# Optimization experiments

Hardware: AMD Instinct MI355X
Metric: run time of the kernel (lower is better)

## Reference

```python
import jax, jax.numpy as jnp
import numpy as np

N_HEAD = 12

def setup_inputs() -> dict:
    key = jax.random.key(0)
    ks = jax.random.split(key, 5)
    B, T, C = 2, 2048, 768
    s = 0.02
    return {
        "x": jax.random.normal(ks[0], (B, T, C), jnp.float32),
        "c_attn_w": jax.random.normal(ks[1], (C, 3 * C), jnp.float32) * s,
        "c_attn_b": jax.random.normal(ks[2], (3 * C,), jnp.float32) * s,
        "c_proj_w": jax.random.normal(ks[3], (C, C), jnp.float32) * s,
        "c_proj_b": jax.random.normal(ks[4], (C,), jnp.float32) * s,
    }

def reference(x, c_attn_w, c_attn_b, c_proj_w, c_proj_b):
    B, T, C = x.shape
    H = N_HEAD
    D = C // H
    qkv = x @ c_attn_w + c_attn_b              # [B,T,3C]
    q, k, v = jnp.split(qkv, 3, axis=-1)
    # [B,T,C] -> [B,H,T,D]
    q = q.reshape(B, T, H, D).transpose(0, 2, 1, 3)
    k = k.reshape(B, T, H, D).transpose(0, 2, 1, 3)
    v = v.reshape(B, T, H, D).transpose(0, 2, 1, 3)
    att = jnp.einsum('bhqd,bhkd->bhqk', q, k) * (1.0 / np.sqrt(D))
    causal = jnp.tril(jnp.ones((T, T), bool))  # [T,T]
    att = jnp.where(causal[None, None], att, jnp.float32(-jnp.inf))
    att = jax.nn.softmax(att, axis=-1)
    y = jnp.einsum('bhqk,bhkd->bhqd', att, v)  # [B,H,T,D]
    y = y.transpose(0, 2, 1, 3).reshape(B, T, C)
    return y @ c_proj_w + c_proj_b
```

## Files before the change

kernel.cpp:

```cpp
#include <hip/hip_runtime.h>
#include <hip/hip_bf16.h>


using half4   = __attribute__((ext_vector_type(4))) _Float16;
using half8   = __attribute__((ext_vector_type(8))) _Float16;
using floatx4 = __attribute__((ext_vector_type(4))) float;

#define T_SEQ 2048
#define NHEAD 12
#define HDIM 64
#define C3 2304
#define CDIM 768
#define BT 4096
#define BH 24

static __device__ inline _Float16 f2h(float f) { return (_Float16)f; }

static __device__ inline void bar_lgkm() {
    __builtin_amdgcn_s_waitcnt(0xc07f);
    __builtin_amdgcn_s_barrier();
}

__global__ __launch_bounds__(256)
void prologue(const float* __restrict__ wa, const float* __restrict__ wp,
              _Float16* __restrict__ wTa, _Float16* __restrict__ wTp) {
    __shared__ float tile[32][33];
    int blk = blockIdx.x, tid = threadIdx.x;
    const float* w; _Float16* wT; int K, N, bx, by;
    if (blk < 1728) { w = wa; wT = wTa; K = CDIM; N = C3; bx = blk % 72; by = blk / 72; }
    else { int b2 = blk - 1728; w = wp; wT = wTp; K = CDIM; N = CDIM; bx = b2 % 24; by = b2 / 24; }
    int tx = tid & 31, ty = tid >> 5;
    #pragma unroll
    for (int j = 0; j < 32; j += 8) {
        int k = by * 32 + ty + j, n = bx * 32 + tx;
        tile[ty + j][tx] = w[(long)k * N + n];
    }
    __syncthreads();
    #pragma unroll
    for (int j = 0; j < 32; j += 8) {
        int nO = bx * 32 + ty + j, kO = by * 32 + tx;
        wT[(long)nO * K + kO] = f2h(tile[tx][ty + j]);
    }
}

__global__ __launch_bounds__(256)
void gemm_qkv(const float* __restrict__ X, const _Float16* __restrict__ Bt,
              const float* __restrict__ bias,
              _Float16* __restrict__ Qb, _Float16* __restrict__ Kb,
              _Float16* __restrict__ Vt) {
    __shared__ __align__(16) _Float16 As[128 * 72];
    __shared__ __align__(16) _Float16 Bs[96 * 72];
    const int K = CDIM;
    int tid = threadIdx.x;
    int m0 = blockIdx.x * 128, n0 = blockIdx.y * 96;
    int w = tid >> 6, l = tid & 63;
    int wm = (w >> 1) * 64, wn = (w & 1) * 48;
    int lr = l & 15, lq = l >> 4;

    int rs = tid >> 3, cs = (tid & 7) * 8;

    floatx4 acc[4][3] = {};

    floatx4 Arf[4][2]; half8 Br[3];
    #pragma unroll
    for (int j = 0; j < 4; ++j) {
        Arf[j][0] = *(const floatx4*)&X[(long)(m0 + j * 32 + rs) * K + cs];
        Arf[j][1] = *(const floatx4*)&X[(long)(m0 + j * 32 + rs) * K + cs + 4];
    }
    #pragma unroll
    for (int j = 0; j < 3; ++j)
        Br[j] = *(const half8*)&Bt[(long)(n0 + j * 32 + rs) * K + cs];

    for (int kb = 0; kb < K; kb += 64) {
        #pragma unroll
        for (int j = 0; j < 4; ++j) {
            half8 h;
            #pragma unroll
            for (int e = 0; e < 4; ++e) { h[e] = f2h(Arf[j][0][e]); h[4 + e] = f2h(Arf[j][1][e]); }
            *(half8*)&As[(j * 32 + rs) * 72 + cs] = h;
        }
        #pragma unroll
        for (int j = 0; j < 3; ++j)
            *(half8*)&Bs[(j * 32 + rs) * 72 + cs] = Br[j];
        bar_lgkm();
        if (kb + 64 < K) {
            #pragma unroll
            for (int j = 0; j < 4; ++j) {
                Arf[j][0] = *(const floatx4*)&X[(long)(m0 + j * 32 + rs) * K + kb + 64 + cs];
                Arf[j][1] = *(const floatx4*)&X[(long)(m0 + j * 32 + rs) * K + kb + 64 + cs + 4];
            }
            #pragma unroll
            for (int j = 0; j < 3; ++j)
                Br[j] = *(const half8*)&Bt[(long)(n0 + j * 32 + rs) * K + kb + 64 + cs];
        }
        #pragma unroll
        for (int kh = 0; kh < 2; ++kh) {
            half8 af[4], bf[3];
            #pragma unroll
            for (int i = 0; i < 4; ++i)
                af[i] = *(const half8*)&As[(wm + i * 16 + lr) * 72 + kh * 32 + lq * 8];
            #pragma unroll
            for (int i = 0; i < 3; ++i)
                bf[i] = *(const half8*)&Bs[(wn + i * 16 + lr) * 72 + kh * 32 + lq * 8];
            #pragma unroll
            for (int mi = 0; mi < 4; ++mi)
                #pragma unroll
                for (int ni = 0; ni < 3; ++ni)
                    acc[mi][ni] = __builtin_amdgcn_mfma_f32_16x16x32_f16(af[mi], bf[ni], acc[mi][ni], 0, 0, 0);
        }
        bar_lgkm();
    }

    int region = n0 / CDIM;
    if (region < 2) {
        _Float16* O = region ? Kb : Qb;
        int nc0 = n0 - region * CDIM + wn;
        #pragma unroll
        for (int mi = 0; mi < 4; ++mi)
            #pragma unroll
            for (int ni = 0; ni < 3; ++ni) {
                int col = nc0 + ni * 16 + lr;
                float bsc = bias[region * CDIM + col];
                #pragma unroll
                for (int r = 0; r < 4; ++r) {
                    int row = m0 + wm + mi * 16 + lq * 4 + r;
                    O[(long)row * CDIM + col] = f2h(acc[mi][ni][r] + bsc);
                }
            }
    } else {
        #pragma unroll
        for (int mi = 0; mi < 4; ++mi)
            #pragma unroll
            for (int ni = 0; ni < 3; ++ni) {
                int cv = n0 - 2 * CDIM + wn + ni * 16 + lr;
                float bsc = bias[2 * CDIM + cv];
                int h = cv >> 6, d = cv & 63;
                int t0 = m0 + wm + mi * 16 + lq * 4;
                int bb = t0 >> 11, t = t0 & 2047;
                half4 hv;
                #pragma unroll
                for (int r = 0; r < 4; ++r) hv[r] = f2h(acc[mi][ni][r] + bsc);
                *(half4*)&Vt[(((long)bb * NHEAD + h) * HDIM + d) * T_SEQ + t] = hv;
            }
    }
}

__global__ __launch_bounds__(256)
void gemm_proj(const _Float16* __restrict__ A, const _Float16* __restrict__ Bt,
               const float* __restrict__ bias, float* __restrict__ Cout) {
    __shared__ __align__(16) _Float16 As[64 * 72];
    __shared__ __align__(16) _Float16 Bs[96 * 72];
    const int K = CDIM, N = CDIM;
    int tid = threadIdx.x;
    int m0 = blockIdx.x * 64, n0 = blockIdx.y * 96;
    int w = tid >> 6, l = tid & 63;
    int wm = (w >> 1) * 32, wn = (w & 1) * 48;
    int lr = l & 15, lq = l >> 4;

    int rs = tid >> 3, cs = (tid & 7) * 8;

    floatx4 acc[2][3] = {};

    half8 Ar[2], Br[3];
    #pragma unroll
    for (int j = 0; j < 2; ++j)
        Ar[j] = *(const half8*)&A[(long)(m0 + j * 32 + rs) * K + cs];
    #pragma unroll
    for (int j = 0; j < 3; ++j)
        Br[j] = *(const half8*)&Bt[(long)(n0 + j * 32 + rs) * K + cs];

    for (int kb = 0; kb < K; kb += 64) {
        #pragma unroll
        for (int j = 0; j < 2; ++j)
            *(half8*)&As[(j * 32 + rs) * 72 + cs] = Ar[j];
        #pragma unroll
        for (int j = 0; j < 3; ++j)
            *(half8*)&Bs[(j * 32 + rs) * 72 + cs] = Br[j];
        bar_lgkm();
        if (kb + 64 < K) {
            #pragma unroll
            for (int j = 0; j < 2; ++j)
                Ar[j] = *(const half8*)&A[(long)(m0 + j * 32 + rs) * K + kb + 64 + cs];
            #pragma unroll
            for (int j = 0; j < 3; ++j)
                Br[j] = *(const half8*)&Bt[(long)(n0 + j * 32 + rs) * K + kb + 64 + cs];
        }
        #pragma unroll
        for (int kh = 0; kh < 2; ++kh) {
            half8 af[2], bf[3];
            #pragma unroll
            for (int i = 0; i < 2; ++i)
                af[i] = *(const half8*)&As[(wm + i * 16 + lr) * 72 + kh * 32 + lq * 8];
            #pragma unroll
            for (int i = 0; i < 3; ++i)
                bf[i] = *(const half8*)&Bs[(wn + i * 16 + lr) * 72 + kh * 32 + lq * 8];
            #pragma unroll
            for (int mi = 0; mi < 2; ++mi)
                #pragma unroll
                for (int ni = 0; ni < 3; ++ni)
                    acc[mi][ni] = __builtin_amdgcn_mfma_f32_16x16x32_f16(af[mi], bf[ni], acc[mi][ni], 0, 0, 0);
        }
        bar_lgkm();
    }
    #pragma unroll
    for (int mi = 0; mi < 2; ++mi)
        #pragma unroll
        for (int ni = 0; ni < 3; ++ni) {
            int col = n0 + wn + ni * 16 + lr;
            float b = bias[col];
            #pragma unroll
            for (int r = 0; r < 4; ++r) {
                int row = m0 + wm + mi * 16 + lq * 4 + r;
                Cout[(long)row * N + col] = acc[mi][ni][r] + b;
            }
        }
}

__global__ __launch_bounds__(256)
void attn_kernel(const _Float16* __restrict__ Qb, const _Float16* __restrict__ Kb,
                 const _Float16* __restrict__ Vt, _Float16* __restrict__ y) {
    __shared__ __align__(16) _Float16 Ks[128 * 72];
    __shared__ __align__(16) _Float16 Vs[64 * 136];
    int tid = threadIdx.x;
    int w = tid >> 6, l = tid & 63;
    int lr = l & 15, lq = l >> 4;
    int qs = (w & 1) * 32;
    int kh2 = (w >> 1) * 64;
    int i = blockIdx.x;
    int round = i >> 8, c = i & 255;
    int r_ = (round == 0) ? c : (round == 1 ? 767 - c : 256 + c);
    int qb = 31 - r_ / 24;
    int bh = r_ % 24;
    int b = bh / NHEAD, h = bh % NHEAD;

    const _Float16* Qp = Qb + (long)b * T_SEQ * CDIM + h * HDIM;
    const _Float16* Kg = Kb + (long)b * T_SEQ * CDIM + h * HDIM;
    const _Float16* Vg = Vt + (long)bh * HDIM * T_SEQ;

    int kr = tid >> 3, kc = (tid & 7) * 8;
    int vr = tid >> 4, vc = (tid & 15) * 8;
    int vpc = (vc & ~31) + ((vc >> 3) & 1) * 16 + ((vc >> 4) & 1) * 4;

    const float qscale = 0.125f * 1.44269504f;
    half8 aq[2][2];
    #pragma unroll
    for (int st = 0; st < 2; ++st)
        #pragma unroll
        for (int kk = 0; kk < 2; ++kk) {
            aq[st][kk] = *(const half8*)&Qp[(long)(qb * 64 + qs + st * 16 + lr) * CDIM + kk * 32 + lq * 8];
            #pragma unroll
            for (int j = 0; j < 8; ++j) aq[st][kk][j] = f2h((float)aq[st][kk][j] * qscale);
        }

    int nk = (qb + 2) >> 1;

    half8 Kr[4], Vr[4];
    #pragma unroll
    for (int j = 0; j < 4; ++j) {
        Kr[j] = *(const half8*)&Kg[(long)(j * 32 + kr) * CDIM + kc];
        Vr[j] = *(const half8*)&Vg[(long)(j * 16 + vr) * T_SEQ + vc];
    }

    float psum[2] = {0.f, 0.f};
    floatx4 acc[4][2] = {};
    int qrow0 = qb * 64 + qs + lr, qrow1 = qb * 64 + qs + 16 + lr;

    for (int kt = 0; kt < nk; ++kt) {
        int kbase = kt * 128;
        #pragma unroll
        for (int j = 0; j < 4; ++j) {
            *(half8*)&Ks[(j * 32 + kr) * 72 + kc] = Kr[j];
            half4 lo, hi;
            #pragma unroll
            for (int e = 0; e < 4; ++e) { lo[e] = Vr[j][e]; hi[e] = Vr[j][4 + e]; }
            *(half4*)&Vs[(j * 16 + vr) * 136 + vpc] = lo;
            *(half4*)&Vs[(j * 16 + vr) * 136 + vpc + 8] = hi;
        }
        bar_lgkm();
        if (kt + 1 < nk) {
            int nb = kbase + 128;
            #pragma unroll
            for (int j = 0; j < 4; ++j) {
                Kr[j] = *(const half8*)&Kg[(long)(nb + j * 32 + kr) * CDIM + kc];
                Vr[j] = *(const half8*)&Vg[(long)(j * 16 + vr) * T_SEQ + nb + vc];
            }
        }

        floatx4 sacc[4][2];
        #pragma unroll
        for (int s = 0; s < 4; ++s)
            #pragma unroll
            for (int st = 0; st < 2; ++st) sacc[s][st] = floatx4{0.f, 0.f, 0.f, 0.f};
        #pragma unroll
        for (int s = 0; s < 4; ++s) {
            #pragma unroll
            for (int kk = 0; kk < 2; ++kk) {
                half8 bk = *(const half8*)&Ks[(kh2 + s * 16 + lr) * 72 + kk * 32 + lq * 8];
                sacc[s][0] = __builtin_amdgcn_mfma_f32_16x16x32_f16(bk, aq[0][kk], sacc[s][0], 0, 0, 0);
                sacc[s][1] = __builtin_amdgcn_mfma_f32_16x16x32_f16(bk, aq[1][kk], sacc[s][1], 0, 0, 0);
            }
        }

        half4 ph[2][4];
        if (kt == nk - 1) {
            #pragma unroll
            for (int s = 0; s < 4; ++s)
                #pragma unroll
                for (int r = 0; r < 4; ++r) {
                    int key = kbase + kh2 + s * 16 + lq * 4 + r;
                    float p0 = (key > qrow0) ? 0.f : __builtin_amdgcn_exp2f(sacc[s][0][r]);
                    float p1 = (key > qrow1) ? 0.f : __builtin_amdgcn_exp2f(sacc[s][1][r]);
                    psum[0] += p0; psum[1] += p1;
                    ph[0][s][r] = f2h(p0); ph[1][s][r] = f2h(p1);
                }
        } else {
            #pragma unroll
            for (int s = 0; s < 4; ++s)
                #pragma unroll
                for (int r = 0; r < 4; ++r) {
                    float p0 = __builtin_amdgcn_exp2f(sacc[s][0][r]);
                    float p1 = __builtin_amdgcn_exp2f(sacc[s][1][r]);
                    psum[0] += p0; psum[1] += p1;
                    ph[0][s][r] = f2h(p0); ph[1][s][r] = f2h(p1);
                }
        }

        #pragma unroll
        for (int kk = 0; kk < 2; ++kk) {
            half8 bp0, bp1;
            #pragma unroll
            for (int e = 0; e < 4; ++e) {
                bp0[e] = ph[0][2 * kk][e];     bp0[4 + e] = ph[0][2 * kk + 1][e];
                bp1[e] = ph[1][2 * kk][e];     bp1[4 + e] = ph[1][2 * kk + 1][e];
            }
            #pragma unroll
            for (int n = 0; n < 4; ++n) {
                half8 av = *(const half8*)&Vs[(n * 16 + lr) * 136 + kh2 + kk * 32 + lq * 8];
                acc[n][0] = __builtin_amdgcn_mfma_f32_16x16x32_f16(av, bp0, acc[n][0], 0, 0, 0);
                acc[n][1] = __builtin_amdgcn_mfma_f32_16x16x32_f16(av, bp1, acc[n][1], 0, 0, 0);
            }
        }
        bar_lgkm();
    }

    float* red = (float*)Ks;
    int slot = ((w & 1) * 64 + l) * 36;
    if (w >= 2) {
        #pragma unroll
        for (int n = 0; n < 4; ++n)
            #pragma unroll
            for (int st = 0; st < 2; ++st)
                *(floatx4*)&red[slot + (n * 2 + st) * 4] = acc[n][st];
        red[slot + 32] = psum[0];
        red[slot + 33] = psum[1];
    }
    __syncthreads();
    if (w < 2) {
        #pragma unroll
        for (int n = 0; n < 4; ++n)
            #pragma unroll
            for (int st = 0; st < 2; ++st) {
                floatx4 t = *(const floatx4*)&red[slot + (n * 2 + st) * 4];
                acc[n][st][0] += t[0]; acc[n][st][1] += t[1];
                acc[n][st][2] += t[2]; acc[n][st][3] += t[3];
            }
        psum[0] += red[slot + 32];
        psum[1] += red[slot + 33];

        #pragma unroll
        for (int st = 0; st < 2; ++st) {
            float L = psum[st];
            L += __shfl_xor(L, 16, 64);
            L += __shfl_xor(L, 32, 64);
            float inv = 1.f / L;
            #pragma unroll
            for (int n = 0; n < 4; ++n) {
                half4 hv;
                #pragma unroll
                for (int r = 0; r < 4; ++r) hv[r] = f2h(acc[n][st][r] * inv);
                int row = qb * 64 + qs + st * 16 + lr;
                *(half4*)&y[((long)(b * T_SEQ) + row) * CDIM + h * HDIM + n * 16 + lq * 4] = hv;
            }
        }
    }
}

extern "C" void kernel_launch(void* const* d_in, const int* in_sizes, int n_in,
                              void* d_out, int out_size, void* d_ws, size_t ws_size,
                              hipStream_t stream) {
    const float* x      = (const float*)d_in[0];
    const float* w_attn = (const float*)d_in[1];
    const float* b_attn = (const float*)d_in[2];
    const float* w_proj = (const float*)d_in[3];
    const float* b_proj = (const float*)d_in[4];
    float* out = (float*)d_out;

    char* ws = (char*)d_ws;
    _Float16* wTa = (_Float16*)(ws + 6291456);
    _Float16* wTp = (_Float16*)(ws + 9830400);
    _Float16* Qb  = (_Float16*)(ws + 11010048);
    _Float16* Kb  = (_Float16*)(ws + 17301504);
    _Float16* Vt  = (_Float16*)(ws + 23592960);
    _Float16* yb  = (_Float16*)(ws + 29884416);

    prologue<<<2304, 256, 0, stream>>>(w_attn, w_proj, wTa, wTp);

    gemm_qkv<<<dim3(BT / 128, C3 / 96), 256, 0, stream>>>(x, wTa, b_attn, Qb, Kb, Vt);

    attn_kernel<<<BH * (T_SEQ / 64), 256, 0, stream>>>(Qb, Kb, Vt, yb);

    gemm_proj<<<dim3(BT / 64, CDIM / 96), 256, 0, stream>>>(yb, wTp, b_proj, out);
}
```

Baseline: 139.3 us.

## Read K directly from global memory and double-buffer V in shared memory

Drops the shared-memory K staging: each wave now loads its K fragments straight from global memory inside the QK^T loop. V is double-buffered in LDS, with the next tile written after the PV MFMAs, so each iteration needs one barrier instead of two. This removes LDS traffic and a barrier, but puts uncached global-load latency directly in front of the score MFMAs. It also duplicates K reads, since the two waves sharing a key half each load the same rows.

```diff
diff --git a/kernel.cpp b/kernel.cpp
--- a/kernel.cpp
+++ b/kernel.cpp
@@ -219,8 +219,7 @@
 __global__ __launch_bounds__(256)
 void attn_kernel(const _Float16* __restrict__ Qb, const _Float16* __restrict__ Kb,
                  const _Float16* __restrict__ Vt, _Float16* __restrict__ y) {
-    __shared__ __align__(16) _Float16 Ks[128 * 72];
-    __shared__ __align__(16) _Float16 Vs[64 * 136];
+    __shared__ __align__(16) _Float16 Vs[2][64 * 136];
     int tid = threadIdx.x;
     int w = tid >> 6, l = tid & 63;
     int lr = l & 15, lq = l >> 4;
@@ -237,7 +236,6 @@
     const _Float16* Kg = Kb + (long)b * T_SEQ * CDIM + h * HDIM;
     const _Float16* Vg = Vt + (long)bh * HDIM * T_SEQ;
 
-    int kr = tid >> 3, kc = (tid & 7) * 8;
     int vr = tid >> 4, vc = (tid & 15) * 8;
     int vpc = (vc & ~31) + ((vc >> 3) & 1) * 16 + ((vc >> 4) & 1) * 4;
 
@@ -254,12 +252,22 @@
 
     int nk = (qb + 2) >> 1;
 
-    half8 Kr[4], Vr[4];
+    _Float16* vs_cur = &Vs[0][0];
+    _Float16* vs_nxt = &Vs[1][0];
+
+    half8 Vr[4];
+    #pragma unroll
+    for (int j = 0; j < 4; ++j)
+        Vr[j] = *(const half8*)&Vg[(long)(j * 16 + vr) * T_SEQ + vc];
     #pragma unroll
     for (int j = 0; j < 4; ++j) {
-        Kr[j] = *(const half8*)&Kg[(long)(j * 32 + kr) * CDIM + kc];
-        Vr[j] = *(const half8*)&Vg[(long)(j * 16 + vr) * T_SEQ + vc];
-    }
+        half4 lo, hi;
+        #pragma unroll
+        for (int e = 0; e < 4; ++e) { lo[e] = Vr[j][e]; hi[e] = Vr[j][4 + e]; }
+        *(half4*)&vs_cur[(j * 16 + vr) * 136 + vpc] = lo;
+        *(half4*)&vs_cur[(j * 16 + vr) * 136 + vpc + 8] = hi;
+    }
+    bar_lgkm();
 
     float psum[2] = {0.f, 0.f};
     floatx4 acc[4][2] = {};
@@ -267,23 +275,11 @@
 
     for (int kt = 0; kt < nk; ++kt) {
         int kbase = kt * 128;
-        #pragma unroll
-        for (int j = 0; j < 4; ++j) {
-            *(half8*)&Ks[(j * 32 + kr) * 72 + kc] = Kr[j];
-            half4 lo, hi;
-            #pragma unroll
-            for (int e = 0; e < 4; ++e) { lo[e] = Vr[j][e]; hi[e] = Vr[j][4 + e]; }
-            *(half4*)&Vs[(j * 16 + vr) * 136 + vpc] = lo;
-            *(half4*)&Vs[(j * 16 + vr) * 136 + vpc + 8] = hi;
-        }
-        bar_lgkm();
         if (kt + 1 < nk) {
             int nb = kbase + 128;
             #pragma unroll
-            for (int j = 0; j < 4; ++j) {
-                Kr[j] = *(const half8*)&Kg[(long)(nb + j * 32 + kr) * CDIM + kc];
+            for (int j = 0; j < 4; ++j)
                 Vr[j] = *(const half8*)&Vg[(long)(j * 16 + vr) * T_SEQ + nb + vc];
-            }
         }
 
         floatx4 sacc[4][2];
@@ -295,7 +291,7 @@
         for (int s = 0; s < 4; ++s) {
             #pragma unroll
             for (int kk = 0; kk < 2; ++kk) {
-                half8 bk = *(const half8*)&Ks[(kh2 + s * 16 + lr) * 72 + kk * 32 + lq * 8];
+                half8 bk = *(const half8*)&Kg[(long)(kbase + kh2 + s * 16 + lr) * CDIM + kk * 32 + lq * 8];
                 sacc[s][0] = __builtin_amdgcn_mfma_f32_16x16x32_f16(bk, aq[0][kk], sacc[s][0], 0, 0, 0);
                 sacc[s][1] = __builtin_amdgcn_mfma_f32_16x16x32_f16(bk, aq[1][kk], sacc[s][1], 0, 0, 0);
             }
@@ -335,15 +331,27 @@
             }
             #pragma unroll
             for (int n = 0; n < 4; ++n) {
-                half8 av = *(const half8*)&Vs[(n * 16 + lr) * 136 + kh2 + kk * 32 + lq * 8];
+                half8 av = *(const half8*)&vs_cur[(n * 16 + lr) * 136 + kh2 + kk * 32 + lq * 8];
                 acc[n][0] = __builtin_amdgcn_mfma_f32_16x16x32_f16(av, bp0, acc[n][0], 0, 0, 0);
                 acc[n][1] = __builtin_amdgcn_mfma_f32_16x16x32_f16(av, bp1, acc[n][1], 0, 0, 0);
             }
         }
+
+        if (kt + 1 < nk) {
+            #pragma unroll
+            for (int j = 0; j < 4; ++j) {
+                half4 lo, hi;
+                #pragma unroll
+                for (int e = 0; e < 4; ++e) { lo[e] = Vr[j][e]; hi[e] = Vr[j][4 + e]; }
+                *(half4*)&vs_nxt[(j * 16 + vr) * 136 + vpc] = lo;
+                *(half4*)&vs_nxt[(j * 16 + vr) * 136 + vpc + 8] = hi;
+            }
+        }
         bar_lgkm();
-    }
-
-    float* red = (float*)Ks;
+        _Float16* tmp = vs_cur; vs_cur = vs_nxt; vs_nxt = tmp;
+    }
+
+    float* red = (float*)&Vs[0][0];
     int slot = ((w & 1) * 64 + l) * 36;
     if (w >= 2) {
         #pragma unroll
```

New measurement: 150.6 us. 1.08x slower.
